# Optimization experiments

Hardware: AMD Instinct MI355X
Metric: run time of the kernel (lower is better)

## Reference

```python
import jax, jax.numpy as jnp
import numpy as np

B, S, HID = 2, 2048, 2048
H, KVH, D = 16, 4, 128
GROUPS = H // KVH  # 4


def apply_rotary(x, cos, sin):
    # x: [B, h, S, D]; cos/sin: [S, D//2]
    xr = x[..., 0::2]
    xi = x[..., 1::2]
    c = cos[None, None, :, :]
    s = sin[None, None, :, :]
    orr = xr * c - xi * s
    oi = xr * s + xi * c
    return jnp.stack([orr, oi], axis=-1).reshape(x.shape)


def setup_inputs() -> dict:
    key = jax.random.key(0)
    k0, k1, k2, k3, k4 = jax.random.split(key, 5)
    x = jax.random.normal(k0, (B, S, HID), dtype=jnp.float32)
    # real RoPE frequencies (llama-style), stored as [S, D//2, 2] = (cos, sin)
    inv_freq = 1.0 / (10000.0 ** (np.arange(0, D, 2, dtype=np.float32) / D))
    t = np.arange(S, dtype=np.float32)
    ang = np.outer(t, inv_freq)  # [S, D//2]
    freqs_cis = jnp.asarray(np.stack([np.cos(ang), np.sin(ang)], axis=-1), dtype=jnp.float32)
    sc = 0.02
    wq = jax.random.normal(k1, (HID, H * D), dtype=jnp.float32) * sc
    wk = jax.random.normal(k2, (HID, KVH * D), dtype=jnp.float32) * sc
    wv = jax.random.normal(k3, (HID, KVH * D), dtype=jnp.float32) * sc
    wo = jax.random.normal(k4, (H * D, HID), dtype=jnp.float32) * sc
    return {"x": x, "freqs_cis": freqs_cis, "wq": wq, "wk": wk, "wv": wv, "wo": wo}


def reference(x, freqs_cis, wq, wk, wv, wo):
    b, s, _ = x.shape
    cos, sin = freqs_cis[..., 0], freqs_cis[..., 1]
    q = (x @ wq).reshape(b, s, H, D).transpose(0, 2, 1, 3)    # [B,H,S,D]
    k = (x @ wk).reshape(b, s, KVH, D).transpose(0, 2, 1, 3)  # [B,KVH,S,D]
    v = (x @ wv).reshape(b, s, KVH, D).transpose(0, 2, 1, 3)
    q = apply_rotary(q, cos, sin)
    k = apply_rotary(k, cos, sin)
    # GQA expand: repeat kv heads into query-head groups
    k = jnp.repeat(k, GROUPS, axis=1)  # [B,H,S,D]
    v = jnp.repeat(v, GROUPS, axis=1)
    scale = 1.0 / jnp.sqrt(jnp.asarray(D, dtype=x.dtype))
    scores = jnp.einsum("bhqd,bhkd->bhqk", q, k) * scale
    causal = jnp.tril(jnp.ones((s, s), dtype=bool))
    scores = jnp.where(causal[None, None], scores, jnp.asarray(-jnp.inf, dtype=scores.dtype))
    attn = jax.nn.softmax(scores, axis=-1)
    out = jnp.einsum("bhqk,bhkd->bhqd", attn, v)
    out = out.transpose(0, 2, 1, 3).reshape(b, s, H * D)
    return out @ wo
```

## Files before the change

### kernel.cpp

```cpp
#include <hip/hip_runtime.h>
#include <hip/hip_bf16.h>

#define B_   2
#define S_   2048
#define HID_ 2048
#define H_   16
#define KVH_ 4
#define D_   128
#define M_   4096
#define NQKV 3072

typedef __attribute__((ext_vector_type(8))) short bf16x8;
typedef __attribute__((ext_vector_type(4))) float f32x4;
typedef const __attribute__((address_space(1))) unsigned int* gas_p;
typedef __attribute__((address_space(3))) unsigned int* las_p;

__device__ __forceinline__ unsigned short f2b(float f) {
    __hip_bfloat16 h = __float2bfloat16(f);
    return *reinterpret_cast<unsigned short*>(&h);
}
__device__ __forceinline__ float b2f(unsigned short u) {
    __hip_bfloat16 h;
    *reinterpret_cast<unsigned short*>(&h) = u;
    return __bfloat162float(h);
}

__global__ __launch_bounds__(256)
void convert_all(const float* __restrict__ x,
                 const float* __restrict__ wq, const float* __restrict__ wk,
                 const float* __restrict__ wv, const float* __restrict__ wo,
                 unsigned short* __restrict__ xb,
                 unsigned short* __restrict__ wqkvT,
                 unsigned short* __restrict__ woT) {
    int z = blockIdx.z;
    if (z >= 4) {
        int lin = ((z - 4) * 64 + blockIdx.y) * 64 + blockIdx.x;
        int i = (lin * 256 + threadIdx.x) * 4;
        float4 v = *(const float4*)(x + i);
        ushort4 o;
        o.x = f2b(v.x); o.y = f2b(v.y); o.z = f2b(v.z); o.w = f2b(v.w);
        *(ushort4*)(xb + i) = o;
        return;
    }
    __shared__ float tile[32][33];
    const float* w; int N, nbase; unsigned short* dst;
    if (z == 0)      { w = wq; N = 2048; nbase = 0;    dst = wqkvT; }
    else if (z == 1) { w = wk; N = 512;  nbase = 2048; dst = wqkvT; }
    else if (z == 2) { w = wv; N = 512;  nbase = 2560; dst = wqkvT; }
    else             { w = wo; N = 2048; nbase = 0;    dst = woT; }
    int n0 = blockIdx.x * 32, k0 = blockIdx.y * 32;
    if (n0 >= N) return;
    int tx = threadIdx.x & 31, ty = threadIdx.x >> 5;
    #pragma unroll
    for (int j = 0; j < 4; j++)
        tile[ty + j*8][tx] = w[(size_t)(k0 + ty + j*8) * N + n0 + tx];
    __syncthreads();
    #pragma unroll
    for (int j = 0; j < 4; j++)
        dst[(size_t)(nbase + n0 + ty + j*8) * 2048 + k0 + tx] = f2b(tile[tx][ty + j*8]);
}

#define BAR    asm volatile("s_barrier" ::: "memory")
#define LG0    do { asm volatile("s_waitcnt lgkmcnt(0)" ::: "memory"); \
                    __builtin_amdgcn_sched_barrier(0); } while (0)
#define GATE0  asm volatile("s_waitcnt vmcnt(0)" ::: "memory")
#define GATE4  asm volatile("s_waitcnt vmcnt(4)" ::: "memory")
#define GATE6  asm volatile("s_waitcnt vmcnt(6)" ::: "memory")
#define GATE7  asm volatile("s_waitcnt vmcnt(7)" ::: "memory")
#define PHI    __builtin_amdgcn_s_setprio(1)
#define PLO    __builtin_amdgcn_s_setprio(0)

#define STG(srcrow, ldsbase, half, tile) do {                                   \
    _Pragma("unroll")                                                           \
    for (int it_ = 0; it_ < 2; ++it_) {                                         \
      int p_ = w * 128 + it_ * 64 + lane;                                       \
      int r_ = (half) * 128 + (p_ >> 3);                                        \
      int q8_ = ((p_ & 7) ^ ((p_ >> 3) & 7)) * 8;                               \
      __builtin_amdgcn_global_load_lds(                                         \
          (gas_p)((srcrow) + (size_t)r_ * 2048 + (tile) * 64 + q8_),            \
          (las_p)((char*)(ldsbase) + ((half) * 1024 + w * 128 + it_ * 64) * 16),\
          16, 0, 0);                                                            \
    } } while (0)

#define STGB(srcrow, ldsbase, unit, tile) do {                                  \
      int p_ = w * 64 + lane;                                                   \
      int r_ = (unit) * 64 + (p_ >> 3);                                         \
      int q8_ = ((p_ & 7) ^ ((p_ >> 3) & 7)) * 8;                               \
      __builtin_amdgcn_global_load_lds(                                         \
          (gas_p)((srcrow) + (size_t)r_ * 2048 + (tile) * 64 + q8_),            \
          (las_p)((char*)(ldsbase) + ((unit) * 512 + p_) * 16),                 \
          16, 0, 0);                                                            \
    } while (0)

#define RDAq(dst, bufi) do {                                                    \
    const unsigned short* Ab_ = &As[bufi][0] + wr*4096 + l15*64;                \
    _Pragma("unroll")                                                           \
    for (int f_ = 0; f_ < 4; ++f_) {                                            \
      dst[f_][0] = *(const bf16x8*)(Ab_ + f_*1024 + slot0);                     \
      dst[f_][1] = *(const bf16x8*)(Ab_ + f_*1024 + slot1);                     \
    } } while (0)

#define RDBq(dst, bufi, nh) do {                                                \
    const unsigned short* Bb_ = &Bs[bufi][0] + wc*6144 + (nh)*3072 + l15*64;    \
    _Pragma("unroll")                                                           \
    for (int g_ = 0; g_ < 3; ++g_) {                                            \
      dst[g_][0] = *(const bf16x8*)(Bb_ + g_*1024 + slot0);                     \
      dst[g_][1] = *(const bf16x8*)(Bb_ + g_*1024 + slot1);                     \
    } } while (0)

#define MMq(mh, rb, nh) do {                                                    \
    _Pragma("unroll")                                                           \
    for (int f_ = 2*(mh); f_ < 2*(mh)+2; ++f_)                                  \
      _Pragma("unroll")                                                         \
      for (int g_ = 0; g_ < 3; ++g_) {                                          \
        acc[f_][(nh)*3+g_] = __builtin_amdgcn_mfma_f32_16x16x32_bf16(           \
            ra[f_][0], rb[g_][0], acc[f_][(nh)*3+g_], 0, 0, 0);                 \
        acc[f_][(nh)*3+g_] = __builtin_amdgcn_mfma_f32_16x16x32_bf16(           \
            ra[f_][1], rb[g_][1], acc[f_][(nh)*3+g_], 0, 0, 0);                 \
      } } while (0)

__global__ __launch_bounds__(512)
void gemm8(const unsigned short* __restrict__ A,
           const unsigned short* __restrict__ BT,
           unsigned short* __restrict__ qkvb,
           unsigned short* __restrict__ vTb,
           const float* __restrict__ freqs) {
    __shared__ unsigned short As[2][16384];
    __shared__ unsigned short Bs[2][12288];

    int tid  = threadIdx.x;
    int lane = tid & 63, w = tid >> 6;
    int l15  = lane & 15, quad = lane >> 4;
    int wr = w >> 1, wc = w & 1;
    int bid = blockIdx.y * 16 + blockIdx.x;
    int s_  = (bid & 7) * 32 + (bid >> 3);
    int by  = s_ >> 4, bx = s_ & 15;
    int row0 = by * 256, col0 = bx * 192;
    int slot0 = (quad ^ (lane & 7)) * 8;
    int slot1 = slot0 ^ 32;

    const unsigned short* Arow = A  + (size_t)row0 * 2048;
    const unsigned short* Brow = BT + (size_t)col0 * 2048;

    f32x4 acc[4][6];
    #pragma unroll
    for (int i = 0; i < 4; ++i)
        #pragma unroll
        for (int j = 0; j < 6; ++j) acc[i][j] = f32x4{0.f, 0.f, 0.f, 0.f};

    bf16x8 ra[4][2];
    bf16x8 rbl[3][2];
    bf16x8 rbh[3][2];

    STG (Arow, &As[0][0], 0, 0);
    STG (Arow, &As[0][0], 1, 0);
    STGB(Brow, &Bs[0][0], 0, 0);
    STGB(Brow, &Bs[0][0], 1, 0);
    STGB(Brow, &Bs[0][0], 2, 0);
    STG (Arow, &As[1][0], 0, 1);
    STG (Arow, &As[1][0], 1, 1);
    STGB(Brow, &Bs[1][0], 0, 1);
    STGB(Brow, &Bs[1][0], 1, 1);
    STGB(Brow, &Bs[1][0], 2, 1);
    GATE7;
    BAR;

    #pragma unroll 1
    for (int i = 0; i < 15; ++i) {
        int t = 2 * i;
        RDAq(ra, 0); RDBq(rbl, 0, 0);
        BAR; LG0; PHI; MMq(0, rbl, 0); PLO; BAR;
        RDBq(rbh, 0, 1); STG(Arow, &As[0][0], 0, t + 2);
        BAR; LG0; PHI; MMq(0, rbh, 1); PLO; BAR;
        STG(Arow, &As[0][0], 1, t + 2);
        BAR; LG0; PHI; MMq(1, rbl, 0); PLO; BAR;
        STGB(Brow, &Bs[0][0], 0, t + 2);
        STGB(Brow, &Bs[0][0], 1, t + 2);
        STGB(Brow, &Bs[0][0], 2, t + 2);
        BAR; LG0; PHI; MMq(1, rbh, 1); PLO; GATE7; BAR;
        RDAq(ra, 1); RDBq(rbl, 1, 0);
        BAR; LG0; PHI; MMq(0, rbl, 0); PLO; BAR;
        RDBq(rbh, 1, 1); STG(Arow, &As[1][0], 0, t + 3);
        BAR; LG0; PHI; MMq(0, rbh, 1); PLO; BAR;
        STG(Arow, &As[1][0], 1, t + 3);
        BAR; LG0; PHI; MMq(1, rbl, 0); PLO; BAR;
        STGB(Brow, &Bs[1][0], 0, t + 3);
        STGB(Brow, &Bs[1][0], 1, t + 3);
        STGB(Brow, &Bs[1][0], 2, t + 3);
        BAR; LG0; PHI; MMq(1, rbh, 1); PLO; GATE7; BAR;
    }
    RDAq(ra, 0); RDBq(rbl, 0, 0);
    BAR; LG0; PHI; MMq(0, rbl, 0); PLO; BAR;
    RDBq(rbh, 0, 1);
    BAR; LG0; PHI; MMq(0, rbh, 1); PLO; BAR;
    BAR; LG0; PHI; MMq(1, rbl, 0); PLO; BAR;
    BAR; LG0; PHI; MMq(1, rbh, 1); PLO; GATE0; BAR;
    RDAq(ra, 1); RDBq(rbl, 1, 0);
    BAR; LG0; PHI; MMq(0, rbl, 0); PLO; BAR;
    RDBq(rbh, 1, 1);
    BAR; LG0; PHI; MMq(0, rbh, 1); PLO; BAR;
    BAR; LG0; PHI; MMq(1, rbl, 0); PLO; BAR;
    LG0; PHI; MMq(1, rbh, 1); PLO;

    int q4 = quad * 4;
    const float qscale = 0.08838834764831845f;
    #pragma unroll
    for (int f = 0; f < 4; ++f) {
        int mb = row0 + wr*64 + f*16 + q4;
        #pragma unroll
        for (int g = 0; g < 6; ++g) {
            int colbase = col0 + wc*96 + g*16;
            int colb = colbase + l15;
            if (colbase < 2560) {
                int dd = (colb & 127) & ~1;
                bool odd = colb & 1;
                float sc = (colbase < 2048) ? qscale : 1.f;
                #pragma unroll
                for (int rr = 0; rr < 4; ++rr) {
                    int m = mb + rr;
                    int s = m & 2047;
                    float v  = acc[f][g][rr];
                    float pv = __shfl_xor(v, 1);
                    float cs = freqs[s*128 + dd];
                    float sn = freqs[s*128 + dd + 1];
                    float o  = odd ? (pv*sn + v*cs) : (v*cs - pv*sn);
                    qkvb[(size_t)m * NQKV + colb] = f2b(o * sc);
                }
            } else {
                int vrow = (row0 >> 11) * 512 + (colb - 2560);
                int s0 = mb & 2047;
                ushort4 ov;
                ov.x = f2b(acc[f][g][0]);
                ov.y = f2b(acc[f][g][1]);
                ov.z = f2b(acc[f][g][2]);
                ov.w = f2b(acc[f][g][3]);
                *(ushort4*)(vTb + (size_t)vrow * 2048 + s0) = ov;
            }
        }
    }
}

#define RDAo(bufi) do {                                                         \
    const unsigned short* Ab_ = &As[bufi][0] + wr * 4096 + l15 * 64;            \
    _Pragma("unroll")                                                           \
    for (int f_ = 0; f_ < 4; ++f_) {                                            \
      af[f_][0] = *(const bf16x8*)(Ab_ + f_ * 1024 + slot0);                    \
      af[f_][1] = *(const bf16x8*)(Ab_ + f_ * 1024 + slot1);                    \
    } } while (0)

#define RDBo(bufi, g) do {                                                      \
    const unsigned short* Bb_ = &Bs[bufi][0] + wc * 4096 + l15 * 64;            \
    bfr[g][0] = *(const bf16x8*)(Bb_ + (g) * 1024 + slot0);                     \
    bfr[g][1] = *(const bf16x8*)(Bb_ + (g) * 1024 + slot1);                     \
    } while (0)

#define MM8o(mi, ni) do {                                                       \
    _Pragma("unroll")                                                           \
    for (int f_ = 2*(mi); f_ < 2*(mi)+2; ++f_)                                  \
      _Pragma("unroll")                                                         \
      for (int g_ = 2*(ni); g_ < 2*(ni)+2; ++g_) {                              \
        acc[f_][g_] = __builtin_amdgcn_mfma_f32_16x16x32_bf16(                  \
            af[f_][0], bfr[g_][0], acc[f_][g_], 0, 0, 0);                       \
        acc[f_][g_] = __builtin_amdgcn_mfma_f32_16x16x32_bf16(                  \
            af[f_][1], bfr[g_][1], acc[f_][g_], 0, 0, 0);                       \
      } } while (0)

__global__ __launch_bounds__(512)
void gemm8o(const unsigned short* __restrict__ A,
            const unsigned short* __restrict__ BT,
            float* __restrict__ Cf) {
    __shared__ unsigned short As[2][16384];
    __shared__ unsigned short Bs[2][8192];

    int tid  = threadIdx.x;
    int lane = tid & 63, w = tid >> 6;
    int l15  = lane & 15, quad = lane >> 4;
    int wr = w >> 1, wc = w & 1;
    int bid = blockIdx.y * 16 + blockIdx.x;
    int s_  = (bid & 7) * 32 + (bid >> 3);
    int by  = s_ >> 4, bx = s_ & 15;
    int row0 = by * 256, col0 = bx * 128;
    int slot0 = (quad ^ (lane & 7)) * 8;
    int slot1 = slot0 ^ 32;

    const unsigned short* Arow = A  + (size_t)row0 * 2048;
    const unsigned short* Brow = BT + (size_t)col0 * 2048;

    f32x4 acc[4][4];
    #pragma unroll
    for (int i = 0; i < 4; ++i)
        #pragma unroll
        for (int j = 0; j < 4; ++j) acc[i][j] = f32x4{0.f, 0.f, 0.f, 0.f};

    bf16x8 af[4][2];
    bf16x8 bfr[4][2];

    STG(Arow, &As[0][0], 0, 0);
    STG(Arow, &As[0][0], 1, 0);
    STG(Brow, &Bs[0][0], 0, 0);
    STG(Arow, &As[1][0], 0, 1);
    STG(Arow, &As[1][0], 1, 1);
    STG(Brow, &Bs[1][0], 0, 1);
    GATE6;
    BAR;

    #pragma unroll 1
    for (int i = 0; i < 15; ++i) {
        int t = 2 * i;
        RDAo(0); RDBo(0, 0); RDBo(0, 1);
        BAR; LG0; PHI; MM8o(0, 0); PLO; BAR;
        RDBo(0, 2); RDBo(0, 3); STG(Arow, &As[0][0], 0, t + 2);
        BAR; LG0; PHI; MM8o(0, 1); PLO; BAR;
        STG(Arow, &As[0][0], 1, t + 2);
        BAR; LG0; PHI; MM8o(1, 0); PLO; BAR;
        STG(Brow, &Bs[0][0], 0, t + 2);
        BAR; LG0; PHI; MM8o(1, 1); PLO; GATE6; BAR;
        RDAo(1); RDBo(1, 0); RDBo(1, 1);
        BAR; LG0; PHI; MM8o(0, 0); PLO; BAR;
        RDBo(1, 2); RDBo(1, 3); STG(Arow, &As[1][0], 0, t + 3);
        BAR; LG0; PHI; MM8o(0, 1); PLO; BAR;
        STG(Arow, &As[1][0], 1, t + 3);
        BAR; LG0; PHI; MM8o(1, 0); PLO; BAR;
        STG(Brow, &Bs[1][0], 0, t + 3);
        BAR; LG0; PHI; MM8o(1, 1); PLO; GATE6; BAR;
    }
    RDAo(0); RDBo(0, 0); RDBo(0, 1);
    BAR; LG0; PHI; MM8o(0, 0); PLO; BAR;
    RDBo(0, 2); RDBo(0, 3);
    BAR; LG0; PHI; MM8o(0, 1); PLO; BAR;
    BAR; LG0; PHI; MM8o(1, 0); PLO; BAR;
    BAR; LG0; PHI; MM8o(1, 1); PLO; GATE0; BAR;
    RDAo(1); RDBo(1, 0); RDBo(1, 1);
    BAR; LG0; PHI; MM8o(0, 0); PLO; BAR;
    RDBo(1, 2); RDBo(1, 3);
    BAR; LG0; PHI; MM8o(0, 1); PLO; BAR;
    BAR; LG0; PHI; MM8o(1, 0); PLO; BAR;
    LG0; PHI; MM8o(1, 1); PLO;

    int q4 = quad * 4;
    #pragma unroll
    for (int f = 0; f < 4; ++f) {
        int mb = row0 + wr*64 + f*16 + q4;
        #pragma unroll
        for (int g = 0; g < 4; ++g) {
            int colb = col0 + wc*64 + g*16 + l15;
            #pragma unroll
            for (int rr = 0; rr < 4; ++rr)
                Cf[(size_t)(mb + rr) * 2048 + colb] = acc[f][g][rr];
        }
    }
}

__global__ __launch_bounds__(512)
void attn_mfma(const unsigned short* __restrict__ qkv,
               const unsigned short* __restrict__ vT,
               unsigned short* __restrict__ ao,
               unsigned short* __restrict__ wsP,
               float2* __restrict__ wsML) {
    __shared__ unsigned short Ks[2][64 * 128];
    __shared__ unsigned short Vt[2][128 * 64];

    int tid  = threadIdx.x;
    int lane = tid & 63, w = tid >> 6;
    int quad = lane >> 4, l15 = lane & 15;
    int hw = w >> 1, qhalf = w & 1;
    int bx = blockIdx.x, hk = blockIdx.y, b = blockIdx.z;
    int h = hk * 4 + hw;

    int qt, c;
    if (bx < 12)      { qt = 31 - bx / 3;        c = bx % 3; }
    else if (bx < 40) { qt = 27 - (bx - 12) / 2; c = (bx - 12) & 1; }
    else              { qt = 53 - bx;            c = 0; }
    int nt = qt + 1;
    int nch = (qt >= 28) ? 3 : (qt >= 14 ? 2 : 1);
    int kt_begin = c * 14;
    int kt_end = (nt < (c + 1) * 14) ? nt : (c + 1) * 14;
    bool lastc = (c == nch - 1);
    int q0 = qt * 64;

    bf16x8 aq[2][4];
    #pragma unroll
    for (int qf = 0; qf < 2; qf++) {
        const unsigned short* qrow =
            qkv + (size_t)(b*2048 + q0 + qhalf*32 + qf*16 + l15) * NQKV + h*128;
        #pragma unroll
        for (int k4 = 0; k4 < 4; k4++)
            aq[qf][k4] = *(const bf16x8*)(qrow + k4*32 + quad*8);
    }

    int koff[4][4];
    #pragma unroll
    for (int j = 0; j < 4; j++) {
        int row = ((j >> 1) * 32) + ((l15 >> 2) * 8) + ((j & 1) * 4) + (l15 & 3);
        #pragma unroll
        for (int k4 = 0; k4 < 4; k4++) {
            int slot = (k4 * 4 + quad) ^ (row & 15);
            koff[j][k4] = (row * 16 + slot) * 8;
        }
    }
    int vbase0 = (l15 * 8 + (quad ^ (l15 & 7))) * 8;
    int vbase1 = (l15 * 8 + ((4 + quad) ^ (l15 & 7))) * 8;

    const unsigned short* kb0 = qkv + (size_t)(b*2048) * NQKV + 2048 + hk*128;
    const unsigned short* vb0 = vT + (size_t)(b*512 + hk*128) * 2048;

    auto stage_k = [&](int bf, int kt) {
        #pragma unroll
        for (int it = 0; it < 2; it++) {
            int s = w * 128 + it * 64 + lane;
            int r = s >> 4, qp = s & 15;
            int q = qp ^ (r & 15);
            __builtin_amdgcn_global_load_lds(
                (gas_p)(kb0 + (size_t)(kt*64 + r) * NQKV + q * 8),
                (las_p)((char*)&Ks[bf][0] + (w * 128 + it * 64) * 16),
                16, 0, 0);
        }
    };
    auto stage_v = [&](int bf, int kt) {
        #pragma unroll
        for (int it = 0; it < 2; it++) {
            int s = w * 128 + it * 64 + lane;
            int r = s >> 3, qp = s & 7;
            int q = qp ^ (r & 7);
            __builtin_amdgcn_global_load_lds(
                (gas_p)(vb0 + (size_t)r * 2048 + kt*64 + q * 8),
                (las_p)((char*)&Vt[bf][0] + (w * 128 + it * 64) * 16),
                16, 0, 0);
        }
    };

    f32x4 o_acc[2][8];
    const f32x4 zf = {0.f, 0.f, 0.f, 0.f};
    #pragma unroll
    for (int qf = 0; qf < 2; qf++)
        #pragma unroll
        for (int jn = 0; jn < 8; jn++) o_acc[qf][jn] = zf;
    float m_i[2] = {-1e30f, -1e30f}, l_i[2] = {0.f, 0.f};
    int qglob[2] = {q0 + qhalf*32 + l15, q0 + qhalf*32 + 16 + l15};

    int kt1 = (kt_begin + 1 < kt_end) ? kt_begin + 1 : kt_begin;
    stage_k(0, kt_begin); stage_v(0, kt_begin);
    stage_k(1, kt1);      stage_v(1, kt1);
    GATE4;
    BAR;

    int p = 0;
    for (int kt = kt_begin; kt < kt_end; kt++) {
        f32x4 s_acc[2][4];
        #pragma unroll
        for (int j = 0; j < 4; j++) {
            s_acc[0][j] = zf; s_acc[1][j] = zf;
            #pragma unroll
            for (int k4 = 0; k4 < 4; k4++) {
                bf16x8 ak = *(const bf16x8*)&Ks[p][koff[j][k4]];
                s_acc[0][j] = __builtin_amdgcn_mfma_f32_16x16x32_bf16(ak, aq[0][k4], s_acc[0][j], 0, 0, 0);
                s_acc[1][j] = __builtin_amdgcn_mfma_f32_16x16x32_bf16(ak, aq[1][k4], s_acc[1][j], 0, 0, 0);
            }
        }

        bf16x8 pp[2][2];
        #pragma unroll
        for (int qf = 0; qf < 2; qf++) {
            float sv[4][4];
            #pragma unroll
            for (int j = 0; j < 4; j++)
                #pragma unroll
                for (int r = 0; r < 4; r++)
                    sv[j][r] = s_acc[qf][j][r];
            if (kt == qt) {
                #pragma unroll
                for (int j = 0; j < 4; j++)
                    #pragma unroll
                    for (int r = 0; r < 4; r++) {
                        int sloc = ((j >> 1) * 32) + quad*8 + ((j & 1) * 4) + r;
                        if (kt*64 + sloc > qglob[qf]) sv[j][r] = -1e30f;
                    }
            }
            float mx = sv[0][0];
            #pragma unroll
            for (int j = 0; j < 4; j++)
                #pragma unroll
                for (int r = 0; r < 4; r++) mx = fmaxf(mx, sv[j][r]);
            mx = fmaxf(mx, __shfl_xor(mx, 16));
            mx = fmaxf(mx, __shfl_xor(mx, 32));
            int defer = __all(mx <= m_i[qf] + 8.f);
            float mnew = defer ? m_i[qf] : fmaxf(m_i[qf], mx);
            float rs = 0.f;
            float pexp[4][4];
            #pragma unroll
            for (int j = 0; j < 4; j++)
                #pragma unroll
                for (int r = 0; r < 4; r++) {
                    pexp[j][r] = __expf(sv[j][r] - mnew);
                    rs += pexp[j][r];
                }
            if (!defer) {
                float alpha = __expf(m_i[qf] - mnew);
                l_i[qf] *= alpha;
                #pragma unroll
                for (int jn = 0; jn < 8; jn++)
                    #pragma unroll
                    for (int r = 0; r < 4; r++) o_acc[qf][jn][r] *= alpha;
                m_i[qf] = mnew;
            }
            l_i[qf] += rs;
            #pragma unroll
            for (int r = 0; r < 4; r++) {
                pp[qf][0][r]     = (short)f2b(pexp[0][r]);
                pp[qf][0][r + 4] = (short)f2b(pexp[1][r]);
                pp[qf][1][r]     = (short)f2b(pexp[2][r]);
                pp[qf][1][r + 4] = (short)f2b(pexp[3][r]);
            }
        }

        #pragma unroll
        for (int jn = 0; jn < 8; jn++) {
            bf16x8 av0 = *(const bf16x8*)&Vt[p][jn*1024 + vbase0];
            bf16x8 av1 = *(const bf16x8*)&Vt[p][jn*1024 + vbase1];
            o_acc[0][jn] = __builtin_amdgcn_mfma_f32_16x16x32_bf16(av0, pp[0][0], o_acc[0][jn], 0, 0, 0);
            o_acc[0][jn] = __builtin_amdgcn_mfma_f32_16x16x32_bf16(av1, pp[0][1], o_acc[0][jn], 0, 0, 0);
            o_acc[1][jn] = __builtin_amdgcn_mfma_f32_16x16x32_bf16(av0, pp[1][0], o_acc[1][jn], 0, 0, 0);
            o_acc[1][jn] = __builtin_amdgcn_mfma_f32_16x16x32_bf16(av1, pp[1][1], o_acc[1][jn], 0, 0, 0);
        }

        BAR;
        int ktn = (kt + 2 < kt_end) ? kt + 2 : kt_end - 1;
        stage_k(p, ktn); stage_v(p, ktn);
        GATE4;
        BAR;
        p ^= 1;
    }

    int pi = 0, mi = 0;
    if (qt >= 14) {
        if (qt < 28) { mi = (qt - 14) * 2 + c;       pi = qt - 14; }
        else         { mi = 28 + (qt - 28) * 3 + c;  pi = 14 + (qt - 28) * 2 + c; }
    }
    #pragma unroll
    for (int qf = 0; qf < 2; qf++) {
        float lt = l_i[qf];
        lt += __shfl_xor(lt, 16);
        lt += __shfl_xor(lt, 32);
        float inv = 1.f / lt;
        int q_local = qhalf * 32 + qf * 16 + l15;
        unsigned short* dst;
        if (lastc)
            dst = ao + (size_t)(b*2048 + q0 + q_local) * 2048 + h*128;
        else
            dst = wsP + (size_t)(((pi * 8 + hk * 2 + b) * 4 + hw) * 64 + q_local) * 128;
        #pragma unroll
        for (int jn = 0; jn < 8; jn++) {
            ushort4 ov;
            ov.x = f2b(o_acc[qf][jn][0] * inv);
            ov.y = f2b(o_acc[qf][jn][1] * inv);
            ov.z = f2b(o_acc[qf][jn][2] * inv);
            ov.w = f2b(o_acc[qf][jn][3] * inv);
            *(ushort4*)(dst + jn*16 + quad*4) = ov;
        }
        if (qt >= 14 && quad == 0)
            wsML[(mi * 8 + hk * 2 + b) * 256 + hw * 64 + q_local]
                = make_float2(m_i[qf], lt);
    }
}

__global__ __launch_bounds__(256)
void merge_kernel(unsigned short* __restrict__ ao,
                  const unsigned short* __restrict__ wsP,
                  const float2* __restrict__ wsML) {
    int t = blockIdx.x * 256 + threadIdx.x;
    int d = (t & 15) * 8;
    int h = (t >> 4) & 15;
    int rest = t >> 8;
    int q_off = rest % 1152;
    int b = rest / 1152;
    int q = 896 + q_off;
    int qt = q >> 6, q_local = q & 63;
    int hk = h >> 2, hw = h & 3;
    int nch = (qt >= 28) ? 3 : 2;

    float mv[3], lv[3];
    for (int cc = 0; cc < nch; cc++) {
        int mi = (qt < 28) ? (qt - 14) * 2 + cc : 28 + (qt - 28) * 3 + cc;
        float2 ml = wsML[(mi * 8 + hk * 2 + b) * 256 + hw * 64 + q_local];
        mv[cc] = ml.x; lv[cc] = ml.y;
    }
    float M = mv[0];
    for (int cc = 1; cc < nch; cc++) M = fmaxf(M, mv[cc]);
    float f[3], S = 0.f;
    for (int cc = 0; cc < nch; cc++) { f[cc] = __expf(mv[cc] - M) * lv[cc]; S += f[cc]; }
    float inv = 1.f / S;

    unsigned short* arow = ao + (size_t)(b*2048 + q) * 2048 + h*128 + d;
    float outv[8];
    {
        ushort4 a0 = *(ushort4*)arow, a1 = *(ushort4*)(arow + 4);
        float fl = f[nch-1];
        outv[0] = fl*b2f(a0.x); outv[1] = fl*b2f(a0.y);
        outv[2] = fl*b2f(a0.z); outv[3] = fl*b2f(a0.w);
        outv[4] = fl*b2f(a1.x); outv[5] = fl*b2f(a1.y);
        outv[6] = fl*b2f(a1.z); outv[7] = fl*b2f(a1.w);
    }
    for (int cc = 0; cc < nch - 1; cc++) {
        int pi = (qt < 28) ? (qt - 14) : 14 + (qt - 28) * 2 + cc;
        const unsigned short* prow =
            wsP + (size_t)(((pi * 8 + hk * 2 + b) * 4 + hw) * 64 + q_local) * 128 + d;
        ushort4 p0 = *(const ushort4*)prow, p1 = *(const ushort4*)(prow + 4);
        float fc = f[cc];
        outv[0] += fc*b2f(p0.x); outv[1] += fc*b2f(p0.y);
        outv[2] += fc*b2f(p0.z); outv[3] += fc*b2f(p0.w);
        outv[4] += fc*b2f(p1.x); outv[5] += fc*b2f(p1.y);
        outv[6] += fc*b2f(p1.z); outv[7] += fc*b2f(p1.w);
    }
    ushort4 o0, o1;
    o0.x = f2b(outv[0]*inv); o0.y = f2b(outv[1]*inv);
    o0.z = f2b(outv[2]*inv); o0.w = f2b(outv[3]*inv);
    o1.x = f2b(outv[4]*inv); o1.y = f2b(outv[5]*inv);
    o1.z = f2b(outv[6]*inv); o1.w = f2b(outv[7]*inv);
    *(ushort4*)arow = o0;
    *(ushort4*)(arow + 4) = o1;
}

extern "C" void kernel_launch(void* const* d_in, const int* in_sizes, int n_in,
                              void* d_out, int out_size, void* d_ws, size_t ws_size,
                              hipStream_t stream) {
    const float* x     = (const float*)d_in[0];
    const float* freqs = (const float*)d_in[1];
    const float* wq    = (const float*)d_in[2];
    const float* wk    = (const float*)d_in[3];
    const float* wv    = (const float*)d_in[4];
    const float* wo    = (const float*)d_in[5];
    float* out = (float*)d_out;

    char* ws = (char*)d_ws;
    unsigned short* xbf    = (unsigned short*)(ws);
    unsigned short* aobuf  = (unsigned short*)(ws);
    unsigned short* wqkvT  = (unsigned short*)(ws + (16u<<20));
    unsigned short* woT    = (unsigned short*)(ws + (28u<<20));
    unsigned short* qkvbuf = (unsigned short*)(ws + (36u<<20));
    unsigned short* vTbuf  = (unsigned short*)(ws + (60u<<20));
    unsigned short* wsP  = (unsigned short*)(ws + (16u<<20));
    float2*         wsML = (float2*)(ws + (16u<<20) + 176u*65536u);

    convert_all<<<dim3(64, 64, 6), dim3(256), 0, stream>>>(
        x, wq, wk, wv, wo, xbf, wqkvT, woT);
    gemm8<<<dim3(16, 16), dim3(512), 0, stream>>>(
        xbf, wqkvT, qkvbuf, vTbuf, freqs);
    attn_mfma<<<dim3(54, 4, 2), dim3(512), 0, stream>>>(qkvbuf, vTbuf, aobuf, wsP, wsML);
    merge_kernel<<<2304, dim3(256), 0, stream>>>(aobuf, wsP, wsML);
    gemm8o<<<dim3(2048/128, M_/256), dim3(512), 0, stream>>>(aobuf, woT, out);
}
```

Measured before the change: 292.7 us.

## Fold log2e into Q scale, balance key-tile chunks, reorder attention blocks

Multiplies the Q scale by log2(e) so softmax can use exp2f directly and skip the multiply inside __expf. It also replaces the fixed 14-tile chunk split with an even split of key tiles across chunks, and maps block indices through a lookup table to a new (qtile, chunk) order. The row max is computed as a tree reduction instead of a serial chain. The defer threshold of 8 now applies in the log2 domain, which changes its effective size, and the merge kernel's chunk indexing must still match the new split.

New measurement: 301.9 us. 3.2% more time.

```diff
diff --git a/kernel.cpp b/kernel.cpp
--- a/kernel.cpp
+++ b/kernel.cpp
@@ -203,7 +203,7 @@
     LG0; PHI; MMq(1, rbh, 1); PLO;
 
     int q4 = quad * 4;
-    const float qscale = 0.08838834764831845f;
+    const float qscale = 0.08838834764831845f * 1.4426950408889634f;
     #pragma unroll
     for (int f = 0; f < 4; ++f) {
         int mb = row0 + wr*64 + f*16 + q4;
@@ -351,6 +351,13 @@
     }
 }
 
+__device__ const unsigned char ATTN_QTC[54] = {
+      8,   4, 121,  76, 120,  80, 124,  89,  93,  97, 101,  96, 109,  52,
+    117,  36, 126,  81,  73, 112,  61,  32,  65,  69,  16,  56,   0,  20,
+    116,  72,  84,  40, 125,  85,  88,  44,  92,  48, 100, 105, 108, 104,
+    122,  77,  68, 113, 114, 118,  60,  64,  57,  28,  12,  24
+};
+
 __global__ __launch_bounds__(512)
 void attn_mfma(const unsigned short* __restrict__ qkv,
                const unsigned short* __restrict__ vT,
@@ -367,14 +374,13 @@
     int bx = blockIdx.x, hk = blockIdx.y, b = blockIdx.z;
     int h = hk * 4 + hw;
 
-    int qt, c;
-    if (bx < 12)      { qt = 31 - bx / 3;        c = bx % 3; }
-    else if (bx < 40) { qt = 27 - (bx - 12) / 2; c = (bx - 12) & 1; }
-    else              { qt = 53 - bx;            c = 0; }
+    int code = ATTN_QTC[bx];
+    int qt = code >> 2, c = code & 3;
     int nt = qt + 1;
     int nch = (qt >= 28) ? 3 : (qt >= 14 ? 2 : 1);
-    int kt_begin = c * 14;
-    int kt_end = (nt < (c + 1) * 14) ? nt : (c + 1) * 14;
+    int base = nt / nch, rem = nt % nch;
+    int kt_begin = c * base + (c < rem ? c : rem);
+    int kt_end   = kt_begin + base + (c < rem ? 1 : 0);
     bool lastc = (c == nch - 1);
     int q0 = qt * 64;
 
@@ -476,11 +482,11 @@
                         if (kt*64 + sloc > qglob[qf]) sv[j][r] = -1e30f;
                     }
             }
-            float mx = sv[0][0];
+            float mj[4];
             #pragma unroll
             for (int j = 0; j < 4; j++)
-                #pragma unroll
-                for (int r = 0; r < 4; r++) mx = fmaxf(mx, sv[j][r]);
+                mj[j] = fmaxf(fmaxf(sv[j][0], sv[j][1]), fmaxf(sv[j][2], sv[j][3]));
+            float mx = fmaxf(fmaxf(mj[0], mj[1]), fmaxf(mj[2], mj[3]));
             mx = fmaxf(mx, __shfl_xor(mx, 16));
             mx = fmaxf(mx, __shfl_xor(mx, 32));
             int defer = __all(mx <= m_i[qf] + 8.f);
@@ -491,11 +497,11 @@
             for (int j = 0; j < 4; j++)
                 #pragma unroll
                 for (int r = 0; r < 4; r++) {
-                    pexp[j][r] = __expf(sv[j][r] - mnew);
+                    pexp[j][r] = exp2f(sv[j][r] - mnew);
                     rs += pexp[j][r];
                 }
             if (!defer) {
-                float alpha = __expf(m_i[qf] - mnew);
+                float alpha = exp2f(m_i[qf] - mnew);
                 l_i[qf] *= alpha;
                 #pragma unroll
                 for (int jn = 0; jn < 8; jn++)
@@ -587,7 +593,7 @@
     float M = mv[0];
     for (int cc = 1; cc < nch; cc++) M = fmaxf(M, mv[cc]);
     float f[3], S = 0.f;
-    for (int cc = 0; cc < nch; cc++) { f[cc] = __expf(mv[cc] - M) * lv[cc]; S += f[cc]; }
+    for (int cc = 0; cc < nch; cc++) { f[cc] = exp2f(mv[cc] - M) * lv[cc]; S += f[cc]; }
     float inv = 1.f / S;
 
     unsigned short* arow = ao + (size_t)(b*2048 + q) * 2048 + h*128 + d;
```
